# Performance work log

Measured on AMD Instinct MI355X. Metric: run time of the kernel, lower is better.

The kernel has to match this reference:

```python
import jax, jax.numpy as jnp
import numpy as np

N = 100000   # num_nodes
HID = 128    # hidden_dim
R = 8        # num_rels
L = 2        # num_layers (HGT builds exactly 2 convs for num_layers=2)
H = 4        # heads
D = HID // H # per-head dim
E = 625000   # num edges


def setup_inputs() -> dict:
    key = jax.random.key(0)
    k = jax.random.split(key, 8)
    x = jnp.arange(N, dtype=jnp.int32)
    edge_index = jax.random.randint(k[0], (2, E), 0, N, dtype=jnp.int32)
    edge_type = jax.random.randint(k[1], (E,), 0, R, dtype=jnp.int32)
    s = 1.0 / float(np.sqrt(HID))
    sd = 1.0 / float(np.sqrt(D))
    emb = jax.random.normal(k[2], (N, HID), jnp.float32) * s          # node embedding table
    W_kqv = jax.random.normal(k[3], (L, HID, 3 * HID), jnp.float32) * s  # fused k/q/v projection per layer
    b_kqv = jnp.zeros((L, 3 * HID), jnp.float32)
    Wk = jax.random.normal(k[4], (L, R, H, D, D), jnp.float32) * sd   # per-relation per-head key transform
    Wv = jax.random.normal(k[5], (L, R, H, D, D), jnp.float32) * sd   # per-relation per-head value transform
    p_rel = jnp.ones((L, R, H), jnp.float32)                          # relation prior
    W_out = jax.random.normal(k[6], (L, HID, HID), jnp.float32) * s   # output projection
    b_out = jnp.zeros((L, HID), jnp.float32)
    skip = jnp.ones((L,), jnp.float32)                                # skip gate (pre-sigmoid)
    return {"emb": emb, "W_kqv": W_kqv, "b_kqv": b_kqv, "Wk": Wk, "Wv": Wv,
            "p_rel": p_rel, "W_out": W_out, "b_out": b_out, "skip": skip,
            "x": x, "edge_index": edge_index, "edge_type": edge_type}


def reference(emb, W_kqv, b_kqv, Wk, Wv, p_rel, W_out, b_out, skip, x, edge_index, edge_type):
    h = emb[x]  # [N, HID]
    src, dst = edge_index[0], edge_index[1]
    scale = 1.0 / np.float32(np.sqrt(D))
    for l in range(L):
        kqv = h @ W_kqv[l] + b_kqv[l]                    # [N, 3*HID]
        kk, q, v = jnp.split(kqv, 3, axis=-1)
        kk = kk.reshape(N, H, D)
        q = q.reshape(N, H, D)
        v = v.reshape(N, H, D)
        k_src = kk[src]                                  # [E, H, D] gather
        v_src = v[src]                                   # [E, H, D]
        # per-relation, per-head linear transforms (HGTConv k_rel / v_rel)
        kp = jnp.zeros_like(k_src)
        vp = jnp.zeros_like(v_src)
        for r in range(R):
            m = (edge_type == r)[:, None, None]
            kp = kp + jnp.where(m, jnp.einsum('ehd,hdf->ehf', k_src, Wk[l, r]), 0.0)
            vp = vp + jnp.where(m, jnp.einsum('ehd,hdf->ehf', v_src, Wv[l, r]), 0.0)
        pr = p_rel[l][edge_type]                         # [E, H]
        alpha = (q[dst] * kp).sum(-1) * pr * scale       # [E, H] attention logits
        # segment softmax over incoming edges of each dst node
        amax = jax.ops.segment_max(alpha, dst, num_segments=N)   # [N, H]
        ee = jnp.exp(alpha - amax[dst])
        denom = jax.ops.segment_sum(ee, dst, num_segments=N)     # [N, H]
        w = ee / denom[dst]                              # [E, H]
        aggr = jax.ops.segment_sum(vp * w[..., None], dst, num_segments=N).reshape(N, HID)
        o = jax.nn.gelu(aggr, approximate=False) @ W_out[l] + b_out[l]
        sg = jax.nn.sigmoid(skip[l])
        h = sg * o + (1.0 - sg) * h                      # HGTConv skip gate (in==out channels)
        h = jax.nn.relu(h)                               # dropout = identity (eval mode)
    return h
```

## Files before the change

### kernel.cpp

```cpp
#include <hip/hip_runtime.h>
#include <math.h>

#define NN    100000
#define HIDN  128
#define NHD   4
#define DDIM  32
#define NREL  8
#define NEDGE 625000
#define NB_SCAN ((NN + 255) / 256)
#define WELEM (2 * NREL * NHD * DDIM * DDIM)
#define MBLK_T ((NN + 127) / 128)
#define RGRP   ((MBLK_T + 7) / 8)
#define GKQV_BLOCKS (RGRP * 24)

typedef unsigned short u16;
typedef unsigned int   u32;
typedef __attribute__((ext_vector_type(8))) short bf16x8;
typedef __attribute__((ext_vector_type(4))) float f32x4;

__device__ __forceinline__ float bf2f(u16 u) {
    union { float f; u32 i; } v; v.i = ((u32)u) << 16; return v.f;
}
__device__ __forceinline__ u16 f2bf(float f) {
    u32 x = __float_as_uint(f);
    return (u16)((x + 0x7fffu + ((x >> 16) & 1u)) >> 16);
}
__device__ __forceinline__ float h2f(u16 h) {
    u32 s = ((u32)(h & 0x8000u)) << 16;
    u32 e = (h >> 10) & 0x1F;
    u32 m = h & 0x3FF;
    union { float f; u32 i; } v;
    if (e == 0) {
        float mag = (float)m * 5.9604644775390625e-8f;
        return (h & 0x8000u) ? -mag : mag;
    }
    if (e == 31) { v.i = s | 0x7F800000u | (m << 13); return v.f; }
    v.i = s | ((e + 112u) << 23) | (m << 13);
    return v.f;
}
__device__ __forceinline__ u16 f2h(float f) {
    u32 x = __float_as_uint(f);
    u32 s = (x >> 16) & 0x8000u;
    int e = (int)((x >> 23) & 0xFF) - 127 + 15;
    u32 m = x & 0x7FFFFFu;
    if (((x >> 23) & 0xFF) == 0xFF) return (u16)(s | (m ? 0x7E00u : 0x7C00u));
    if (e >= 31) return (u16)(s | 0x7C00u);
    if (e <= 0) {
        if (e < -10) return (u16)s;
        m |= 0x800000u;
        int sh = 14 - e;
        u32 r = m >> sh, rem = m & ((1u << sh) - 1), half = 1u << (sh - 1);
        r += (rem > half) || ((rem == half) && (r & 1));
        return (u16)(s | r);
    }
    u32 r = m >> 13, rem = m & 0x1FFFu;
    r += (rem > 0x1000u) || ((rem == 0x1000u) && (r & 1));
    return (u16)(s | (((u32)e << 10) + r));
}
__device__ __forceinline__ float load_in(const u16* p, size_t i, int mode) {
    if (mode == 2) return ((const float*)p)[i];
    u16 v = p[i];
    return mode ? bf2f(v) : h2f(v);
}
__device__ __forceinline__ void load8(const u16* p, size_t i, int mode, float* o) {
    if (mode == 2) {
        float4 a = *(const float4*)((const float*)p + i);
        float4 b = *(const float4*)((const float*)p + i + 4);
        o[0]=a.x; o[1]=a.y; o[2]=a.z; o[3]=a.w; o[4]=b.x; o[5]=b.y; o[6]=b.z; o[7]=b.w;
    } else {
        uint4 v = *(const uint4*)(p + i);
        u32 w[4] = {v.x, v.y, v.z, v.w};
#pragma unroll
        for (int j = 0; j < 4; ++j) {
            u16 lo = (u16)(w[j] & 0xFFFFu), hi = (u16)(w[j] >> 16);
            o[2*j]   = mode ? bf2f(lo) : h2f(lo);
            o[2*j+1] = mode ? bf2f(hi) : h2f(hi);
        }
    }
}
__device__ __forceinline__ void loadi8(const u16* p, size_t i, float* o) {
    uint4 v = *(const uint4*)(p + i);
    u32 w[4] = {v.x, v.y, v.z, v.w};
#pragma unroll
    for (int j = 0; j < 4; ++j) {
        o[2*j]   = bf2f((u16)(w[j] & 0xFFFFu));
        o[2*j+1] = bf2f((u16)(w[j] >> 16));
    }
}
__device__ __forceinline__ float gelu_exact(float x) {
    return 0.5f * x * (1.0f + erff(x * 0.70710678118654752f));
}

__global__ void mode_kernel(const u16* __restrict__ skip, int* __restrict__ gmode) {
    if (threadIdx.x == 0) {
        u16 a = skip[0], b = skip[1];
        int m;
        if (a == 0x3C00u) m = 0;
        else if (a == 0x3F80u) m = 1;
        else if (a == 0u && b == 0x3F80u) m = 2;
        else m = 1;
        gmode[0] = m;
    }
}

__global__ __launch_bounds__(256) void convw_all_kernel(
    const u16* __restrict__ Wk, const u16* __restrict__ Wv, const u16* __restrict__ p_rel,
    const u16* __restrict__ Wkqv, const u16* __restrict__ Wout,
    const u16* __restrict__ bkqv, const u16* __restrict__ bout, const u16* __restrict__ skip,
    float* __restrict__ WkT, float* __restrict__ WvT,
    u16* __restrict__ WkTb, u16* __restrict__ WvTb, float* __restrict__ prf,
    u16* __restrict__ WkqvT, u16* __restrict__ WoutT,
    float* __restrict__ biasf, float* __restrict__ skipf,
    const int* __restrict__ gmode) {
    const int mode = gmode[0];
    const int bid = blockIdx.x;
    if (bid < 512) {
        const int tid = bid * 256 + threadIdx.x;
        if (tid < 2 * NREL * NHD) prf[tid] = load_in(p_rel, tid, mode);
        const int i = (tid < WELEM) ? tid : tid - WELEM;
        const int lrh = i >> 10, rem = i & 1023, d = rem >> 5, f = rem & 31;
        const size_t oidx = ((size_t)lrh << 10) + (f << 5) + d;
        if (tid < WELEM) {
            float v = load_in(Wk, (size_t)i, mode);
            WkT[oidx] = v; WkTb[oidx] = f2bf(v);
        } else {
            float v = load_in(Wv, (size_t)i, mode);
            WvT[oidx] = v; WvTb[oidx] = f2bf(v);
        }
    } else {
        const int t = (bid - 512) * 256 + threadIdx.x;
        if (t < 98304) {
            const int l = t / 49152, rem = t % 49152, k = rem / 384, n = rem % 384;
            WkqvT[(size_t)l * 49152 + (size_t)n * 128 + k] = f2bf(load_in(Wkqv, t, mode));
        } else if (t < 131072) {
            const int i = t - 98304;
            const int l = i / 16384, rem = i % 16384, k = rem / 128, n = rem % 128;
            WoutT[(size_t)l * 16384 + (size_t)n * 128 + k] = f2bf(load_in(Wout, i, mode));
        }
        else if (t < 131840)  biasf[t - 131072] = load_in(bkqv, t - 131072, mode);
        else if (t < 132096)  biasf[768 + t - 131840] = load_in(bout, t - 131840, mode);
        else if (t < 132098)  skipf[t - 132096] = load_in(skip, t - 132096, mode);
    }
}

__global__ __launch_bounds__(256) void hist_kernel(const int* __restrict__ ei,
                                                   const int* __restrict__ et,
                                                   int* __restrict__ deg,
                                                   int* __restrict__ rmeta) {
    __shared__ int c[NREL];
    int t = threadIdx.x;
    if (t < NREL) c[t] = 0;
    __syncthreads();
    int e = blockIdx.x * 256 + t;
    if (e < NEDGE) {
        atomicAdd(&deg[ei[NEDGE + e]], 1);
        atomicAdd(&c[et[e]], 1);
    }
    __syncthreads();
    if (t < NREL && c[t]) atomicAdd(&rmeta[t], c[t]);
}
__global__ __launch_bounds__(256) void scan1_kernel(const int* __restrict__ deg,
                                                    int* __restrict__ rowptr,
                                                    int* __restrict__ bsums, int n) {
    __shared__ int sm[256];
    int i = blockIdx.x * 256 + threadIdx.x;
    int t = threadIdx.x;
    sm[t] = (i < n) ? deg[i] : 0;
    __syncthreads();
#pragma unroll
    for (int off = 1; off < 256; off <<= 1) {
        int v = (t >= off) ? sm[t - off] : 0;
        __syncthreads();
        sm[t] += v;
        __syncthreads();
    }
    if (i < n) rowptr[i + 1] = sm[t];
    if (t == 255) bsums[blockIdx.x] = sm[255];
}
__global__ __launch_bounds__(512) void scan2_kernel(int* __restrict__ bsums, int nb,
                                                    int* __restrict__ rmeta) {
    __shared__ int sm[512];
    int t = threadIdx.x;
    sm[t] = (t < nb) ? bsums[t] : 0;
    __syncthreads();
#pragma unroll
    for (int off = 1; off < 512; off <<= 1) {
        int v = (t >= off) ? sm[t - off] : 0;
        __syncthreads();
        sm[t] += v;
        __syncthreads();
    }
    if (t < nb) bsums[t] = (t > 0) ? sm[t - 1] : 0;
    if (t == 0) {
        int b = 0;
        for (int r = 0; r < NREL; ++r) {
            rmeta[8 + r] = b;
            rmeta[16 + r] = b;
            b += rmeta[r];
        }
    }
}
__global__ __launch_bounds__(256) void scan3_kernel(int* __restrict__ rowptr,
                                                    const int* __restrict__ bsums,
                                                    int* __restrict__ pos, int n) {
    int i = blockIdx.x * 256 + threadIdx.x;
    if (i == 0) { rowptr[0] = 0; pos[0] = 0; }
    if (i < n) {
        int v = rowptr[i + 1] + bsums[blockIdx.x];
        rowptr[i + 1] = v;
        if (i + 1 < n) pos[i + 1] = v;
    }
}
__global__ __launch_bounds__(256) void fill_slot_kernel(const int* __restrict__ ei,
                                                        int* __restrict__ pos,
                                                        int* __restrict__ slot) {
    int e = blockIdx.x * 256 + threadIdx.x;
    if (e < NEDGE) slot[e] = atomicAdd(&pos[ei[NEDGE + e]], 1);
}
__global__ __launch_bounds__(256) void fill_eidx_kernel(const int* __restrict__ ei,
                                                        int* __restrict__ pos,
                                                        int* __restrict__ eidx) {
    int e = blockIdx.x * 256 + threadIdx.x;
    if (e < NEDGE) {
        int idx = atomicAdd(&pos[ei[NEDGE + e]], 1);
        eidx[idx] = e;
    }
}
__global__ __launch_bounds__(256) void rfill_kernel(const int* __restrict__ et,
                                                    int* __restrict__ rmeta,
                                                    int* __restrict__ rlist) {
    __shared__ int c[NREL];
    __shared__ int base[NREL];
    int t = threadIdx.x;
    if (t < NREL) c[t] = 0;
    __syncthreads();
    int e = blockIdx.x * 256 + t;
    int r = -1, rank = 0;
    if (e < NEDGE) {
        r = et[e];
        rank = atomicAdd(&c[r], 1);
    }
    __syncthreads();
    if (t < NREL) base[t] = c[t] ? atomicAdd(&rmeta[16 + t], c[t]) : 0;
    __syncthreads();
    if (e < NEDGE) rlist[base[r] + rank] = e;
}

__global__ __launch_bounds__(256) void gemm_kqv_mfma(
    const u16* __restrict__ A, const u16* __restrict__ embp, const int* __restrict__ x,
    const u16* __restrict__ BwT, const float* __restrict__ biasf,
    u16* __restrict__ C, int M, int l, const int* __restrict__ gmode) {
    __shared__ u16 As[128][128];
    const int mode = gmode[0];
    const int t = threadIdx.x;
    const int g = blockIdx.x;
    const int wi = g % 24;
    const int rowt = (g / 24) * 8 + (wi & 7);
    const int ct = wi >> 3;
    const int row0 = rowt * 128;
    {
        const int row = t >> 1, c0 = (t & 1) * 64;
        const int grow = row0 + row;
        const int swz = (row & 7) << 3;
        if (grow < M) {
            if (l == 0) {
                const int nrow = x[grow];
                float tf[8];
#pragma unroll
                for (int j = 0; j < 8; ++j) {
                    load8(embp, (size_t)nrow * 128 + c0 + j * 8, mode, tf);
                    uint4 v;
                    v.x = (u32)f2bf(tf[0]) | ((u32)f2bf(tf[1]) << 16);
                    v.y = (u32)f2bf(tf[2]) | ((u32)f2bf(tf[3]) << 16);
                    v.z = (u32)f2bf(tf[4]) | ((u32)f2bf(tf[5]) << 16);
                    v.w = (u32)f2bf(tf[6]) | ((u32)f2bf(tf[7]) << 16);
                    *(uint4*)&As[row][(c0 + j * 8) ^ swz] = v;
                }
            } else {
                const uint4* src = (const uint4*)(A + (size_t)grow * 128 + c0);
#pragma unroll
                for (int j = 0; j < 8; ++j)
                    *(uint4*)&As[row][(c0 + j * 8) ^ swz] = src[j];
            }
        } else {
            const uint4 z = make_uint4(0, 0, 0, 0);
#pragma unroll
            for (int j = 0; j < 8; ++j)
                *(uint4*)&As[row][(c0 + j * 8) ^ swz] = z;
        }
    }
    __syncthreads();
    const int wid = t >> 6, lane = t & 63;
    const int wm = wid >> 1, wn = wid & 1;
    const int r16 = lane & 15, kg = lane >> 4;
    const int swz = (r16 & 7) << 3;
    const u16* __restrict__ Bb = BwT + (size_t)l * 49152 + (size_t)(ct * 128) * 128;
    f32x4 acc[4][4];
#pragma unroll
    for (int i = 0; i < 4; ++i)
#pragma unroll
        for (int j = 0; j < 4; ++j) acc[i][j] = (f32x4){0.f, 0.f, 0.f, 0.f};
#pragma unroll
    for (int kk = 0; kk < 4; ++kk) {
        const int kb = kk * 32 + kg * 8;
        bf16x8 af[4], bf[4];
#pragma unroll
        for (int mf = 0; mf < 4; ++mf)
            af[mf] = *(const bf16x8*)&As[wm * 64 + mf * 16 + r16][kb ^ swz];
#pragma unroll
        for (int nf = 0; nf < 4; ++nf)
            bf[nf] = *(const bf16x8*)(Bb + (size_t)(wn * 64 + nf * 16 + r16) * 128 + kb);
#pragma unroll
        for (int mf = 0; mf < 4; ++mf)
#pragma unroll
            for (int nf = 0; nf < 4; ++nf)
                acc[mf][nf] = __builtin_amdgcn_mfma_f32_16x16x32_bf16(
                    af[mf], bf[nf], acc[mf][nf], 0, 0, 0);
    }
    __syncthreads();
    u16* __restrict__ Cs = &As[0][0];
#pragma unroll
    for (int mf = 0; mf < 4; ++mf)
#pragma unroll
        for (int nf = 0; nf < 4; ++nf) {
            const int col = wn * 64 + nf * 16 + r16;
            const float bv = biasf[l * 384 + ct * 128 + col];
#pragma unroll
            for (int r = 0; r < 4; ++r) {
                const int row = wm * 64 + mf * 16 + kg * 4 + r;
                Cs[row * 128 + col] = f2bf(acc[mf][nf][r] + bv);
            }
        }
    __syncthreads();
    const int l16 = t & 15, rowg = t >> 4;
#pragma unroll
    for (int rr = 0; rr < 8; ++rr) {
        const int row = rr * 16 + rowg;
        const int grow = row0 + row;
        if (grow < M)
            *(uint4*)(C + (size_t)grow * 384 + ct * 128 + l16 * 8) =
                *(const uint4*)(Cs + row * 128 + l16 * 8);
    }
}

__global__ __launch_bounds__(256) void gemm_out_mfma(
    const u16* __restrict__ A, const u16* __restrict__ BwT, const float* __restrict__ biasf,
    const float* __restrict__ skipf, const u16* __restrict__ hin,
    const u16* __restrict__ embp, const int* __restrict__ x,
    u16* __restrict__ C, int M, int l, int outsel, const int* __restrict__ gmode) {
    __shared__ u16 As[128][128];
    const int mode = gmode[0];
    const int t = threadIdx.x;
    const int row0 = blockIdx.y * 128;
    {
        const int row = t >> 1, c0 = (t & 1) * 64;
        const int grow = row0 + row;
        const int swz = (row & 7) << 3;
        if (grow < M) {
            const uint4* src = (const uint4*)(A + (size_t)grow * 128 + c0);
#pragma unroll
            for (int j = 0; j < 8; ++j)
                *(uint4*)&As[row][(c0 + j * 8) ^ swz] = src[j];
        } else {
            const uint4 z = make_uint4(0, 0, 0, 0);
#pragma unroll
            for (int j = 0; j < 8; ++j)
                *(uint4*)&As[row][(c0 + j * 8) ^ swz] = z;
        }
    }
    __syncthreads();
    const int wid = t >> 6, lane = t & 63;
    const int wm = wid >> 1, wn = wid & 1;
    const int r16 = lane & 15, kg = lane >> 4;
    const int swz = (r16 & 7) << 3;
    const u16* __restrict__ Bb = BwT + (size_t)l * 16384;
    f32x4 acc[4][4];
#pragma unroll
    for (int i = 0; i < 4; ++i)
#pragma unroll
        for (int j = 0; j < 4; ++j) acc[i][j] = (f32x4){0.f, 0.f, 0.f, 0.f};
#pragma unroll
    for (int kk = 0; kk < 4; ++kk) {
        const int kb = kk * 32 + kg * 8;
        bf16x8 af[4], bf[4];
#pragma unroll
        for (int mf = 0; mf < 4; ++mf)
            af[mf] = *(const bf16x8*)&As[wm * 64 + mf * 16 + r16][kb ^ swz];
#pragma unroll
        for (int nf = 0; nf < 4; ++nf)
            bf[nf] = *(const bf16x8*)(Bb + (size_t)(wn * 64 + nf * 16 + r16) * 128 + kb);
#pragma unroll
        for (int mf = 0; mf < 4; ++mf)
#pragma unroll
            for (int nf = 0; nf < 4; ++nf)
                acc[mf][nf] = __builtin_amdgcn_mfma_f32_16x16x32_bf16(
                    af[mf], bf[nf], acc[mf][nf], 0, 0, 0);
    }
    __syncthreads();
    u16* __restrict__ Cs = &As[0][0];
    {
        const int row = t >> 1, c0 = (t & 1) * 64;
        const int grow = row0 + row;
        if (grow < M) {
            if (l == 0) {
                const int nrow = x[grow];
                float tf[8];
#pragma unroll
                for (int j = 0; j < 8; ++j) {
                    load8(embp, (size_t)nrow * 128 + c0 + j * 8, mode, tf);
                    uint4 v;
                    v.x = (u32)f2bf(tf[0]) | ((u32)f2bf(tf[1]) << 16);
                    v.y = (u32)f2bf(tf[2]) | ((u32)f2bf(tf[3]) << 16);
                    v.z = (u32)f2bf(tf[4]) | ((u32)f2bf(tf[5]) << 16);
                    v.w = (u32)f2bf(tf[6]) | ((u32)f2bf(tf[7]) << 16);
                    *(uint4*)&Cs[row * 128 + c0 + j * 8] = v;
                }
            } else {
                const uint4* src = (const uint4*)(hin + (size_t)grow * 128 + c0);
#pragma unroll
                for (int j = 0; j < 8; ++j)
                    *(uint4*)&Cs[row * 128 + c0 + j * 8] = src[j];
            }
        }
    }
    __syncthreads();
    const float sg = 1.0f / (1.0f + expf(-skipf[l]));
    const float omsg = 1.0f - sg;
    const int f32out = (outsel >= 0 && mode == 2);
#pragma unroll
    for (int mf = 0; mf < 4; ++mf)
#pragma unroll
        for (int nf = 0; nf < 4; ++nf) {
            const int col = wn * 64 + nf * 16 + r16;
            const float bv = biasf[768 + l * 128 + col];
#pragma unroll
            for (int r = 0; r < 4; ++r) {
                const int row = wm * 64 + mf * 16 + kg * 4 + r;
                const int grow = row0 + row;
                if (grow >= M) continue;
                const float hvv = bf2f(Cs[row * 128 + col]);
                const float v = fmaxf(sg * (acc[mf][nf][r] + bv) + omsg * hvv, 0.f);
                if (f32out)
                    ((float*)C)[(size_t)grow * 128 + col] = v;
                else if (outsel >= 0 && mode == 0)
                    Cs[row * 128 + col] = f2h(v);
                else
                    Cs[row * 128 + col] = f2bf(v);
            }
        }
    if (!f32out) {
        __syncthreads();
        const int l16 = t & 15, rowg = t >> 4;
#pragma unroll
        for (int rr = 0; rr < 8; ++rr) {
            const int row = rr * 16 + rowg;
            const int grow = row0 + row;
            if (grow < M)
                *(uint4*)(C + (size_t)grow * 128 + l16 * 8) =
                    *(const uint4*)(Cs + row * 128 + l16 * 8);
        }
    }
}

template<int NH>
__global__ __launch_bounds__(256) void edge_mfma_nh(
    const u16* __restrict__ kqv, const u16* __restrict__ WkTb,
    const u16* __restrict__ WvTb, const float* __restrict__ prf,
    const int* __restrict__ ei, const int* __restrict__ rmeta,
    const int* __restrict__ rlist, const int* __restrict__ slot,
    float* __restrict__ evbuf, u16* __restrict__ vptbuf, int l, int h0) {
    const int r  = blockIdx.y;
    const int lane = threadIdx.x & 63;
    const int f = lane & 15, kg = lane >> 4;
    const int cnt = rmeta[r];
    const int rb  = rmeta[8 + r];
    if (cnt == 0) return;
    const int wv  = (blockIdx.x * 256 + threadIdx.x) >> 6;
    const int nwv = gridDim.x * 4;

    float prh[NH];
#pragma unroll
    for (int h = 0; h < NH; ++h)
        prh[h] = prf[(l * NREL + r) * NHD + h0 + h] * 0.17677669529663687f;

    const size_t wbase = (((size_t)(l * NREL + r) * NHD + h0) << 10);
    bf16x8 bk[NH][2], bv[NH][2];
#pragma unroll
    for (int h = 0; h < NH; ++h) {
        const size_t wb = wbase + ((size_t)h << 10);
        bk[h][0] = *(const bf16x8*)(WkTb + wb + (size_t)f * 32 + kg * 8);
        bk[h][1] = *(const bf16x8*)(WkTb + wb + (size_t)(f + 16) * 32 + kg * 8);
        bv[h][0] = *(const bf16x8*)(WvTb + wb + (size_t)f * 32 + kg * 8);
        bv[h][1] = *(const bf16x8*)(WvTb + wb + (size_t)(f + 16) * 32 + kg * 8);
    }

    const int ntile = (cnt + 15) >> 4;
    int tile = wv;
    if (tile >= ntile) return;
    int myi = tile * 16 + f; if (myi >= cnt) myi = cnt - 1;
    int e = rlist[rb + myi];
    int src = ei[e], dst = ei[NEDGE + e], sl = slot[e];
    bf16x8 ak[NH], av[NH];
    float qv[NH][4][2];
    {
        const u16* kvrow = kqv + (size_t)src * 384 + h0 * 32;
#pragma unroll
        for (int h = 0; h < NH; ++h) {
            ak[h] = *(const bf16x8*)(kvrow + h * 32 + kg * 8);
            av[h] = *(const bf16x8*)(kvrow + 256 + h * 32 + kg * 8);
        }
#pragma unroll
        for (int rr = 0; rr < 4; ++rr) {
            const int d2 = __shfl(dst, kg * 4 + rr, 64);
            const u16* qrow = kqv + (size_t)d2 * 384 + 128 + h0 * 32;
#pragma unroll
            for (int h = 0; h < NH; ++h) {
                qv[h][rr][0] = bf2f(qrow[h * 32 + f]);
                qv[h][rr][1] = bf2f(qrow[h * 32 + f + 16]);
            }
        }
    }
#pragma unroll 1
    for (; tile < ntile; ) {
        const int base = tile << 4;
        const int tnext = tile + nwv;
        int e2 = e, src2 = src, dst2 = dst, sl2v = sl;
        bf16x8 ak2[NH], av2[NH];
        float qv2[NH][4][2];
#pragma unroll
        for (int h = 0; h < NH; ++h) { ak2[h] = ak[h]; av2[h] = av[h]; }
#pragma unroll
        for (int rr = 0; rr < 4; ++rr)
#pragma unroll
            for (int h = 0; h < NH; ++h) {
                qv2[h][rr][0] = qv[h][rr][0]; qv2[h][rr][1] = qv[h][rr][1];
            }
        if (tnext < ntile) {
            int myi2 = tnext * 16 + f; if (myi2 >= cnt) myi2 = cnt - 1;
            e2 = rlist[rb + myi2];
            src2 = ei[e2]; dst2 = ei[NEDGE + e2]; sl2v = slot[e2];
            const u16* kvrow2 = kqv + (size_t)src2 * 384 + h0 * 32;
#pragma unroll
            for (int h = 0; h < NH; ++h) {
                ak2[h] = *(const bf16x8*)(kvrow2 + h * 32 + kg * 8);
                av2[h] = *(const bf16x8*)(kvrow2 + 256 + h * 32 + kg * 8);
            }
#pragma unroll
            for (int rr = 0; rr < 4; ++rr) {
                const int d2 = __shfl(dst2, kg * 4 + rr, 64);
                const u16* qrow2 = kqv + (size_t)d2 * 384 + 128 + h0 * 32;
#pragma unroll
                for (int h = 0; h < NH; ++h) {
                    qv2[h][rr][0] = bf2f(qrow2[h * 32 + f]);
                    qv2[h][rr][1] = bf2f(qrow2[h * 32 + f + 16]);
                }
            }
        }
        const f32x4 z = (f32x4){0.f, 0.f, 0.f, 0.f};
        f32x4 ck0[NH], ck1[NH], cv0[NH], cv1[NH];
#pragma unroll
        for (int h = 0; h < NH; ++h) {
            ck0[h] = __builtin_amdgcn_mfma_f32_16x16x32_bf16(ak[h], bk[h][0], z, 0, 0, 0);
            ck1[h] = __builtin_amdgcn_mfma_f32_16x16x32_bf16(ak[h], bk[h][1], z, 0, 0, 0);
            cv0[h] = __builtin_amdgcn_mfma_f32_16x16x32_bf16(av[h], bv[h][0], z, 0, 0, 0);
            cv1[h] = __builtin_amdgcn_mfma_f32_16x16x32_bf16(av[h], bv[h][1], z, 0, 0, 0);
        }
#pragma unroll
        for (int rr = 0; rr < 4; ++rr) {
            const int el = kg * 4 + rr;
            const int sl2 = __shfl(sl, el, 64);
            float evv[NH];
#pragma unroll
            for (int h = 0; h < NH; ++h) {
                float part = qv[h][rr][0] * ck0[h][rr] + qv[h][rr][1] * ck1[h][rr];
                part += __shfl_xor(part, 1, 64);
                part += __shfl_xor(part, 2, 64);
                part += __shfl_xor(part, 4, 64);
                part += __shfl_xor(part, 8, 64);
                evv[h] = expf(part * prh[h]);
            }
            if (base + el < cnt) {
                if (f == rr) {
                    if (NH == 1) evbuf[sl2] = evv[0];
                    else if (NH == 2)
                        *(float2*)(evbuf + (size_t)sl2 * 2) = make_float2(evv[0], evv[NH - 1]);
                    else
                        *(float4*)(evbuf + (size_t)sl2 * 4) =
                            make_float4(evv[0], evv[1 % NH], evv[2 % NH], evv[3 % NH]);
                }
#pragma unroll
                for (int h = 0; h < NH; ++h) {
                    u16* __restrict__ vph = vptbuf + (size_t)h * NEDGE * 32;
                    vph[(size_t)sl2 * 32 + f]      = f2bf(cv0[h][rr]);
                    vph[(size_t)sl2 * 32 + f + 16] = f2bf(cv1[h][rr]);
                }
            }
        }
        tile = tnext; e = e2; src = src2; dst = dst2; sl = sl2v;
#pragma unroll
        for (int h = 0; h < NH; ++h) { ak[h] = ak2[h]; av[h] = av2[h]; }
#pragma unroll
        for (int rr = 0; rr < 4; ++rr)
#pragma unroll
            for (int h = 0; h < NH; ++h) {
                qv[h][rr][0] = qv2[h][rr][0]; qv[h][rr][1] = qv2[h][rr][1];
            }
    }
}

__global__ __launch_bounds__(256) void HGT_67877663146324_kernel(
    const float* __restrict__ evbuf, const u16* __restrict__ vptbuf,
    const int* __restrict__ rowptr, u16* __restrict__ aggrb, int h0, int nhs) {
    const int hz = blockIdx.y;
    const int hh = h0 + hz;
    const int node = blockIdx.x * 4 + (threadIdx.x >> 6);
    const int lane = threadIdx.x & 63;
    const int p = lane & 15;
    const int sub = lane >> 4;
    if (node >= NN) return;
    const int beg = rowptr[node];
    const int end = rowptr[node + 1];
    const u32* __restrict__ vp = (const u32*)(vptbuf + (size_t)hz * NEDGE * 32);
    float S = 0.f, a0 = 0.f, a1 = 0.f;
#pragma unroll 1
    for (int idx = beg + sub; idx < end; idx += 4) {
        const float ev = evbuf[(size_t)idx * nhs + hz];
        const u32 w = vp[(size_t)idx * 16 + p];
        a0 = fmaf(ev, bf2f((u16)(w & 0xFFFFu)), a0);
        a1 = fmaf(ev, bf2f((u16)(w >> 16)), a1);
        S += ev;
    }
    a0 += __shfl_xor(a0, 16, 64); a0 += __shfl_xor(a0, 32, 64);
    a1 += __shfl_xor(a1, 16, 64); a1 += __shfl_xor(a1, 32, 64);
    S  += __shfl_xor(S, 16, 64);  S  += __shfl_xor(S, 32, 64);
    if (sub == 0) {
        const float o0 = (end > beg) ? a0 / S : 0.f;
        const float o1 = (end > beg) ? a1 / S : 0.f;
        const u32 packed = (u32)f2bf(gelu_exact(o0)) | ((u32)f2bf(gelu_exact(o1)) << 16);
        *(u32*)(aggrb + (size_t)node * HIDN + hh * 32 + 2 * p) = packed;
    }
}

__global__ __launch_bounds__(256) void fused_edge_kernel(
    const u16* __restrict__ kqv, const float* __restrict__ WkT,
    const float* __restrict__ WvT, const float* __restrict__ prf,
    const int* __restrict__ ei, const int* __restrict__ et,
    const int* __restrict__ rowptr, const int* __restrict__ eidx,
    u16* __restrict__ aggrb, int l) {
    const int hh = blockIdx.y;
    const int node = blockIdx.x * 8 + (threadIdx.x >> 5);
    const int lane = threadIdx.x & 31;
    if (node >= NN) return;
    const int beg = rowptr[node];
    const int end = rowptr[node + 1];
    const float qf = bf2f(kqv[(size_t)node * 384 + 128 + hh * DDIM + lane]);
    const float* __restrict__ wkb = WkT + (((size_t)l * NREL * NHD) << 10) + ((size_t)lane << 5);
    const float* __restrict__ wvb = WvT + (((size_t)l * NREL * NHD) << 10) + ((size_t)lane << 5);
    const float* __restrict__ prl = prf + l * NREL * NHD;
    float S = 0.f, acc = 0.f;
#pragma unroll 1
    for (int idx = beg; idx < end; ++idx) {
        const int e   = eidx[idx];
        const int src = ei[e];
        const int r   = et[e];
        const size_t woff = ((size_t)(r * NHD + hh)) << 10;
        const u16* kp = kqv + (size_t)src * 384 + hh * DDIM;
        float kd[DDIM];
        loadi8(kp, 0, kd); loadi8(kp, 8, kd + 8);
        loadi8(kp, 16, kd + 16); loadi8(kp, 24, kd + 24);
        const float* wr = wkb + woff;
        float ka = 0.f;
#pragma unroll
        for (int d0 = 0; d0 < DDIM; d0 += 4) {
            float4 w = *(const float4*)(wr + d0);
            ka = fmaf(kd[d0],     w.x, ka);
            ka = fmaf(kd[d0 + 1], w.y, ka);
            ka = fmaf(kd[d0 + 2], w.z, ka);
            ka = fmaf(kd[d0 + 3], w.w, ka);
        }
        float part = qf * ka;
#pragma unroll
        for (int m = 16; m; m >>= 1) part += __shfl_xor(part, m, 32);
        const float a  = part * prl[r * NHD + hh] * 0.17677669529663687f;
        const float ev = expf(a);
        S += ev;
        const u16* vpp = kqv + (size_t)src * 384 + 256 + hh * DDIM;
        float vd[DDIM];
        loadi8(vpp, 0, vd); loadi8(vpp, 8, vd + 8);
        loadi8(vpp, 16, vd + 16); loadi8(vpp, 24, vd + 24);
        const float* wr2 = wvb + woff;
        float va = 0.f;
#pragma unroll
        for (int d0 = 0; d0 < DDIM; d0 += 4) {
            float4 w = *(const float4*)(wr2 + d0);
            va = fmaf(vd[d0],     w.x, va);
            va = fmaf(vd[d0 + 1], w.y, va);
            va = fmaf(vd[d0 + 2], w.z, va);
            va = fmaf(vd[d0 + 3], w.w, va);
        }
        acc = fmaf(ev, va, acc);
    }
    const float o = (end > beg) ? acc / S : 0.f;
    aggrb[(size_t)node * HIDN + hh * DDIM + lane] = f2bf(gelu_exact(o));
}

extern "C" void kernel_launch(void* const* d_in, const int* in_sizes, int n_in,
                              void* d_out, int out_size, void* d_ws, size_t ws_size,
                              hipStream_t stream) {
    (void)n_in;
    const u16* emb   = (const u16*)d_in[0];
    const u16* W_kqv = (const u16*)d_in[1];
    const u16* b_kqv = (const u16*)d_in[2];
    const u16* Wk    = (const u16*)d_in[3];
    const u16* Wv    = (const u16*)d_in[4];
    const u16* p_rel = (const u16*)d_in[5];
    const u16* W_out = (const u16*)d_in[6];
    const u16* b_out = (const u16*)d_in[7];
    const u16* skip  = (const u16*)d_in[8];
    const int* x     = (const int*)d_in[9];
    const int* ei    = (const int*)d_in[10];
    const int* et    = (const int*)d_in[11];

    const size_t NF_KQV  = (size_t)NN * 384 / 2;
    const size_t NF_AGGR = (size_t)NN * HIDN / 2;
    const size_t NF_H1   = (size_t)NN * HIDN / 2;
    const size_t NF_W    = 2 * (size_t)WELEM + 64 + (size_t)WELEM
                         + (98304 + 32768) / 2 + 1024 + 8;
    const size_t NI_COM  = (size_t)(NN + 1) + NN + 64 + 512 + 64 + NEDGE;
    const size_t BASE    = NF_KQV + NF_AGGR + NF_H1 + NF_W + NI_COM + 1024;
    const size_t T1F = BASE + (size_t)NEDGE + 17ull * 1 * NEDGE;
    const size_t T2F = BASE + (size_t)NEDGE + 17ull * 2 * NEDGE;
    const size_t T4F = BASE + (size_t)NEDGE + 17ull * 4 * NEDGE;

    if (ws_size < BASE * sizeof(float)) {
        (void)hipMemsetAsync(d_out, 0x47, (size_t)out_size * sizeof(u16), stream);
        return;
    }
    bool ok = in_sizes[0] == NN * HIDN && in_sizes[1] == 2 * HIDN * 3 * HIDN &&
              in_sizes[9] == NN && in_sizes[10] == 2 * NEDGE && in_sizes[11] == NEDGE &&
              out_size == NN * HIDN;
    if (!ok) {
        (void)hipMemsetAsync(d_out, 0x46, (size_t)out_size * sizeof(u16), stream);
        return;
    }
    int nh = 0;
    if (ws_size >= T4F * sizeof(float))      nh = 4;
    else if (ws_size >= T2F * sizeof(float)) nh = 2;
    else if (ws_size >= T1F * sizeof(float)) nh = 1;

    float* fws    = (float*)d_ws;
    u16*   kqv    = (u16*)fws;
    u16*   aggrb  = (u16*)(fws + NF_KQV);
    u16*   hbuf1  = (u16*)(fws + NF_KQV + NF_AGGR);
    float* WkT    = fws + NF_KQV + NF_AGGR + NF_H1;
    float* WvT    = WkT + WELEM;
    float* prf    = WvT + WELEM;
    u16*   WkTb   = (u16*)(prf + 64);
    u16*   WvTb   = WkTb + WELEM;
    u16*   WkqvT  = WvTb + WELEM;
    u16*   WoutT  = WkqvT + 98304;
    float* biasf  = (float*)(WoutT + 32768);
    float* skipf  = biasf + 1024;
    int*   rowptr = (int*)(skipf + 8);
    int*   degpos = rowptr + (NN + 1);
    int*   rmeta  = degpos + NN;
    int*   bsums  = rmeta + 64;
    int*   gmode  = bsums + 512;
    int*   arrA   = gmode + 64;
    int*   rlist  = arrA + NEDGE;
    float* evbuf  = (float*)(rlist + NEDGE);
    u16*   vptbuf = (u16*)(evbuf + (size_t)(nh > 0 ? nh : 1) * NEDGE);

    const int EBLK = (NEDGE + 255) / 256;
    const int MBLK = MBLK_T;

    mode_kernel<<<1, 64, 0, stream>>>(skip, gmode);
    convw_all_kernel<<<1029, 256, 0, stream>>>(Wk, Wv, p_rel, W_kqv, W_out, b_kqv, b_out, skip,
                                               WkT, WvT, WkTb, WvTb, prf,
                                               WkqvT, WoutT, biasf, skipf, gmode);

    (void)hipMemsetAsync(degpos, 0, (size_t)(NN + 64) * sizeof(int), stream);
    hist_kernel<<<EBLK, 256, 0, stream>>>(ei, et, degpos, rmeta);
    scan1_kernel<<<NB_SCAN, 256, 0, stream>>>(degpos, rowptr, bsums, NN);
    scan2_kernel<<<1, 512, 0, stream>>>(bsums, NB_SCAN, rmeta);
    scan3_kernel<<<NB_SCAN, 256, 0, stream>>>(rowptr, bsums, degpos, NN);
    if (nh > 0) {
        fill_slot_kernel<<<EBLK, 256, 0, stream>>>(ei, degpos, arrA);
        rfill_kernel<<<EBLK, 256, 0, stream>>>(et, rmeta, rlist);
    } else {
        fill_eidx_kernel<<<EBLK, 256, 0, stream>>>(ei, degpos, arrA);
    }

    for (int l = 0; l < 2; ++l) {
        u16* hout  = (l == 0) ? hbuf1 : (u16*)d_out;
        int outsel = (l == 0) ? -1 : 0;

        gemm_kqv_mfma<<<GKQV_BLOCKS, 256, 0, stream>>>(hbuf1, emb, x, WkqvT, biasf,
                                                       kqv, NN, l, gmode);
        if (nh > 0) {
            for (int h0 = 0; h0 < NHD; h0 += nh) {
                if (nh == 4)
                    edge_mfma_nh<4><<<dim3(128, NREL), 256, 0, stream>>>(
                        kqv, WkTb, WvTb, prf, ei, rmeta, rlist, arrA, evbuf, vptbuf, l, h0);
                else if (nh == 2)
                    edge_mfma_nh<2><<<dim3(128, NREL), 256, 0, stream>>>(
                        kqv, WkTb, WvTb, prf, ei, rmeta, rlist, arrA, evbuf, vptbuf, l, h0);
                else
                    edge_mfma_nh<1><<<dim3(128, NREL), 256, 0, stream>>>(
                        kqv, WkTb, WvTb, prf, ei, rmeta, rlist, arrA, evbuf, vptbuf, l, h0);
                HGT_67877663146324_kernel<<<dim3((NN + 3) / 4, nh), 256, 0, stream>>>(
                    evbuf, vptbuf, rowptr, aggrb, h0, nh);
            }
        } else {
            fused_edge_kernel<<<dim3(NN / 8, NHD), 256, 0, stream>>>(
                kqv, WkT, WvT, prf, ei, et, rowptr, arrA, aggrb, l);
        }
        gemm_out_mfma<<<dim3(1, MBLK), 256, 0, stream>>>(aggrb, WoutT, biasf, skipf,
                                                         hbuf1, emb, x,
                                                         hout, NN, l, outsel, gmode);
    }
}
```

Before: 989.8 us.

## Pack per-relation edge records into CSR-sorted int4 and widen edge grid

Builds CSR order first, then groups edges by relation while iterating in CSR-slot order, storing src, dst and slot as one packed int4 record. The edge MFMA kernel loads that single record instead of chasing rlist→ei→slot through three dependent gathers, and edges within each relation now follow destination order, which should improve locality of the q-row gathers and of the evbuf/vptbuf writes. The edge kernel grid grows from 128 to 192 blocks per relation. This costs a larger workspace (4 ints per edge) and one extra dependent read in the preprocessing fill.

```diff
diff --git a/kernel.cpp b/kernel.cpp
--- a/kernel.cpp
+++ b/kernel.cpp
@@ -211,39 +211,35 @@
         if (i + 1 < n) pos[i + 1] = v;
     }
 }
-__global__ __launch_bounds__(256) void fill_slot_kernel(const int* __restrict__ ei,
-                                                        int* __restrict__ pos,
-                                                        int* __restrict__ slot) {
-    int e = blockIdx.x * 256 + threadIdx.x;
-    if (e < NEDGE) slot[e] = atomicAdd(&pos[ei[NEDGE + e]], 1);
-}
-__global__ __launch_bounds__(256) void fill_eidx_kernel(const int* __restrict__ ei,
-                                                        int* __restrict__ pos,
-                                                        int* __restrict__ eidx) {
+__global__ __launch_bounds__(256) void fill_csr_kernel(const int* __restrict__ ei,
+                                                       int* __restrict__ pos,
+                                                       int* __restrict__ eidxc) {
     int e = blockIdx.x * 256 + threadIdx.x;
     if (e < NEDGE) {
-        int idx = atomicAdd(&pos[ei[NEDGE + e]], 1);
-        eidx[idx] = e;
-    }
-}
-__global__ __launch_bounds__(256) void rfill_kernel(const int* __restrict__ et,
-                                                    int* __restrict__ rmeta,
-                                                    int* __restrict__ rlist) {
+        int s = atomicAdd(&pos[ei[NEDGE + e]], 1);
+        eidxc[s] = e;
+    }
+}
+__global__ __launch_bounds__(256) void edata_fill_kernel(
+    const int* __restrict__ ei, const int* __restrict__ et,
+    const int* __restrict__ eidxc, int* __restrict__ rmeta, int4* __restrict__ edata) {
     __shared__ int c[NREL];
     __shared__ int base[NREL];
     int t = threadIdx.x;
     if (t < NREL) c[t] = 0;
     __syncthreads();
-    int e = blockIdx.x * 256 + t;
-    int r = -1, rank = 0;
-    if (e < NEDGE) {
+    int s = blockIdx.x * 256 + t;
+    int r = -1, rank = 0, e = 0;
+    if (s < NEDGE) {
+        e = eidxc[s];
         r = et[e];
         rank = atomicAdd(&c[r], 1);
     }
     __syncthreads();
     if (t < NREL) base[t] = c[t] ? atomicAdd(&rmeta[16 + t], c[t]) : 0;
     __syncthreads();
-    if (e < NEDGE) rlist[base[r] + rank] = e;
+    if (s < NEDGE)
+        edata[base[r] + rank] = make_int4(ei[e], ei[NEDGE + e], s, 0);
 }
 
 __global__ __launch_bounds__(256) void gemm_kqv_mfma(
@@ -466,8 +462,7 @@
 __global__ __launch_bounds__(256) void edge_mfma_nh(
     const u16* __restrict__ kqv, const u16* __restrict__ WkTb,
     const u16* __restrict__ WvTb, const float* __restrict__ prf,
-    const int* __restrict__ ei, const int* __restrict__ rmeta,
-    const int* __restrict__ rlist, const int* __restrict__ slot,
+    const int* __restrict__ rmeta, const int4* __restrict__ edata,
     float* __restrict__ evbuf, u16* __restrict__ vptbuf, int l, int h0) {
     const int r  = blockIdx.y;
     const int lane = threadIdx.x & 63;
@@ -498,8 +493,8 @@
     int tile = wv;
     if (tile >= ntile) return;
     int myi = tile * 16 + f; if (myi >= cnt) myi = cnt - 1;
-    int e = rlist[rb + myi];
-    int src = ei[e], dst = ei[NEDGE + e], sl = slot[e];
+    int4 ed = edata[rb + myi];
+    int src = ed.x, dst = ed.y, sl = ed.z;
     bf16x8 ak[NH], av[NH];
     float qv[NH][4][2];
     {
@@ -524,7 +519,7 @@
     for (; tile < ntile; ) {
         const int base = tile << 4;
         const int tnext = tile + nwv;
-        int e2 = e, src2 = src, dst2 = dst, sl2v = sl;
+        int src2 = src, dst2 = dst, sl2v = sl;
         bf16x8 ak2[NH], av2[NH];
         float qv2[NH][4][2];
 #pragma unroll
@@ -537,8 +532,8 @@
             }
         if (tnext < ntile) {
             int myi2 = tnext * 16 + f; if (myi2 >= cnt) myi2 = cnt - 1;
-            e2 = rlist[rb + myi2];
-            src2 = ei[e2]; dst2 = ei[NEDGE + e2]; sl2v = slot[e2];
+            int4 ed2 = edata[rb + myi2];
+            src2 = ed2.x; dst2 = ed2.y; sl2v = ed2.z;
             const u16* kvrow2 = kqv + (size_t)src2 * 384 + h0 * 32;
 #pragma unroll
             for (int h = 0; h < NH; ++h) {
@@ -596,7 +591,7 @@
                 }
             }
         }
-        tile = tnext; e = e2; src = src2; dst = dst2; sl = sl2v;
+        tile = tnext; src = src2; dst = dst2; sl = sl2v;
 #pragma unroll
         for (int h = 0; h < NH; ++h) { ak[h] = ak2[h]; av[h] = av2[h]; }
 #pragma unroll
@@ -726,11 +721,11 @@
     const size_t NF_H1   = (size_t)NN * HIDN / 2;
     const size_t NF_W    = 2 * (size_t)WELEM + 64 + (size_t)WELEM
                          + (98304 + 32768) / 2 + 1024 + 8;
-    const size_t NI_COM  = (size_t)(NN + 1) + NN + 64 + 512 + 64 + NEDGE;
+    const size_t NI_COM  = (size_t)(NN + 16) + NN + 64 + 512 + 64 + NEDGE;
     const size_t BASE    = NF_KQV + NF_AGGR + NF_H1 + NF_W + NI_COM + 1024;
-    const size_t T1F = BASE + (size_t)NEDGE + 17ull * 1 * NEDGE;
-    const size_t T2F = BASE + (size_t)NEDGE + 17ull * 2 * NEDGE;
-    const size_t T4F = BASE + (size_t)NEDGE + 17ull * 4 * NEDGE;
+    const size_t T1F = BASE + (4ull + 17ull * 1) * NEDGE;
+    const size_t T2F = BASE + (4ull + 17ull * 2) * NEDGE;
+    const size_t T4F = BASE + (4ull + 17ull * 4) * NEDGE;
 
     if (ws_size < BASE * sizeof(float)) {
         (void)hipMemsetAsync(d_out, 0x47, (size_t)out_size * sizeof(u16), stream);
@@ -762,13 +757,13 @@
     float* biasf  = (float*)(WoutT + 32768);
     float* skipf  = biasf + 1024;
     int*   rowptr = (int*)(skipf + 8);
-    int*   degpos = rowptr + (NN + 1);
+    int*   degpos = rowptr + (NN + 16);
     int*   rmeta  = degpos + NN;
     int*   bsums  = rmeta + 64;
     int*   gmode  = bsums + 512;
-    int*   arrA   = gmode + 64;
-    int*   rlist  = arrA + NEDGE;
-    float* evbuf  = (float*)(rlist + NEDGE);
+    int*   eidxc  = gmode + 64;
+    int4*  edata  = (int4*)(eidxc + NEDGE);
+    float* evbuf  = (float*)(edata + NEDGE);
     u16*   vptbuf = (u16*)(evbuf + (size_t)(nh > 0 ? nh : 1) * NEDGE);
 
     const int EBLK = (NEDGE + 255) / 256;
@@ -784,12 +779,9 @@
     scan1_kernel<<<NB_SCAN, 256, 0, stream>>>(degpos, rowptr, bsums, NN);
     scan2_kernel<<<1, 512, 0, stream>>>(bsums, NB_SCAN, rmeta);
     scan3_kernel<<<NB_SCAN, 256, 0, stream>>>(rowptr, bsums, degpos, NN);
-    if (nh > 0) {
-        fill_slot_kernel<<<EBLK, 256, 0, stream>>>(ei, degpos, arrA);
-        rfill_kernel<<<EBLK, 256, 0, stream>>>(et, rmeta, rlist);
-    } else {
-        fill_eidx_kernel<<<EBLK, 256, 0, stream>>>(ei, degpos, arrA);
-    }
+    fill_csr_kernel<<<EBLK, 256, 0, stream>>>(ei, degpos, eidxc);
+    if (nh > 0)
+        edata_fill_kernel<<<EBLK, 256, 0, stream>>>(ei, et, eidxc, rmeta, edata);
 
     for (int l = 0; l < 2; ++l) {
         u16* hout  = (l == 0) ? hbuf1 : (u16*)d_out;
@@ -800,20 +792,20 @@
         if (nh > 0) {
             for (int h0 = 0; h0 < NHD; h0 += nh) {
                 if (nh == 4)
-                    edge_mfma_nh<4><<<dim3(128, NREL), 256, 0, stream>>>(
-                        kqv, WkTb, WvTb, prf, ei, rmeta, rlist, arrA, evbuf, vptbuf, l, h0);
+                    edge_mfma_nh<4><<<dim3(192, NREL), 256, 0, stream>>>(
+                        kqv, WkTb, WvTb, prf, rmeta, edata, evbuf, vptbuf, l, h0);
                 else if (nh == 2)
-                    edge_mfma_nh<2><<<dim3(128, NREL), 256, 0, stream>>>(
-                        kqv, WkTb, WvTb, prf, ei, rmeta, rlist, arrA, evbuf, vptbuf, l, h0);
+                    edge_mfma_nh<2><<<dim3(192, NREL), 256, 0, stream>>>(
+                        kqv, WkTb, WvTb, prf, rmeta, edata, evbuf, vptbuf, l, h0);
                 else
-                    edge_mfma_nh<1><<<dim3(128, NREL), 256, 0, stream>>>(
-                        kqv, WkTb, WvTb, prf, ei, rmeta, rlist, arrA, evbuf, vptbuf, l, h0);
+                    edge_mfma_nh<1><<<dim3(192, NREL), 256, 0, stream>>>(
+                        kqv, WkTb, WvTb, prf, rmeta, edata, evbuf, vptbuf, l, h0);
                 HGT_67877663146324_kernel<<<dim3((NN + 3) / 4, nh), 256, 0, stream>>>(
                     evbuf, vptbuf, rowptr, aggrb, h0, nh);
             }
         } else {
             fused_edge_kernel<<<dim3(NN / 8, NHD), 256, 0, stream>>>(
-                kqv, WkT, WvT, prf, ei, et, rowptr, arrA, aggrb, l);
+                kqv, WkT, WvT, prf, ei, et, rowptr, eidxc, aggrb, l);
         }
         gemm_out_mfma<<<dim3(1, MBLK), 256, 0, stream>>>(aggrb, WoutT, biasf, skipf,
                                                          hbuf1, emb, x,
```

Result: faster. 866.2 us (-12.5%).
